# Performance work log

Hardware: AMD Instinct MI355X
Metric: run time of the kernel (lower is better)

The kernel has to match this reference:

```python
import jax, jax.numpy as jnp
import numpy as np

R_MAX = 5.0
NUM_RADIAL = 8
HIDDEN = 128
MUL1 = HIDDEN // 2  # multiplicity of the 1o irrep (l_max=1)
SILU_2MOM = 1.679177  # e3nn normalize2mom constant for silu
SQRT3 = 3.0 ** 0.5
N_NODES = 50000
N_EDGES = 400000


def setup_inputs():
    key = jax.random.key(0)
    ks = jax.random.split(key, 9)
    node_attrs = jax.random.normal(ks[0], (N_NODES, HIDDEN), jnp.float32)
    edge_index = jax.random.randint(ks[1], (2, N_EDGES), 0, N_NODES, jnp.int32)
    edge_vec = jax.random.normal(ks[2], (N_EDGES, 3), jnp.float32)
    edge_len = jax.random.uniform(ks[3], (N_EDGES,), jnp.float32, 0.05, R_MAX * 0.95)
    W1 = jax.random.normal(ks[4], (NUM_RADIAL, 64), jnp.float32)
    W2 = jax.random.normal(ks[5], (64, HIDDEN), jnp.float32)
    Wtp0 = jax.random.normal(ks[6], (HIDDEN, HIDDEN), jnp.float32)  # 0e x 0e -> 0e path weights
    Wtp1 = jax.random.normal(ks[7], (HIDDEN, MUL1), jnp.float32)   # 0e x 1o -> 1o path weights
    Wmix0 = jax.random.normal(ks[8], (HIDDEN + MUL1, HIDDEN), jnp.float32)  # o3.Linear 0e->0e
    return dict(node_attrs=node_attrs, edge_index=edge_index, edge_vec=edge_vec,
                edge_len=edge_len, W1=W1, W2=W2, Wtp0=Wtp0, Wtp1=Wtp1, Wmix0=Wmix0)


def _ace_forward(node_attrs, edge_vec, edge_len, W1, W2, Wtp0, Wtp1, Wmix0, sender, receiver):
    N = node_attrs.shape[0]
    # --- bessel radial basis with cutoff (e3nn soft_one_hot_linspace, basis='bessel') ---
    roots = jnp.arange(1, NUM_RADIAL + 1, dtype=node_attrs.dtype) * jnp.pi
    x = edge_len[:, None]
    rad = jnp.sqrt(2.0 / R_MAX) * jnp.sin(roots * x / R_MAX) / x        # [E, num_radial]
    rad = rad * (((edge_len > 0.0) & (edge_len < R_MAX)).astype(rad.dtype))[:, None]
    # --- radial MLP (e3nn FullyConnectedNet: W/sqrt(fan_in), 2nd-moment-normalized silu) ---
    h = SILU_2MOM * jax.nn.silu(rad @ (W1 / np.sqrt(NUM_RADIAL)))
    R_n = h @ (W2 / np.sqrt(64.0))                                       # [E, H]
    # --- spherical harmonics l<=1, normalize=True, 'component' norm; e3nn l=1 order (y,z,x) ---
    unit = edge_vec / jnp.linalg.norm(edge_vec, axis=-1, keepdims=True)
    Y1 = SQRT3 * unit[:, jnp.array([1, 2, 0])]                           # [E, 3]; Y0 == 1
    # --- gather + radial gating ---
    node_feats = node_attrs[sender] * R_n                                # [E, H]
    # --- FullyConnectedTensorProduct: Hx0e (x) (1x0e+1x1o) -> Hx0e + (H/2)x1o ---
    # effective coefficient per path: alpha * w3j = 1/sqrt(fan_in) = 1/sqrt(H)
    inv = 1.0 / np.sqrt(HIDDEN)
    f0 = (node_feats @ Wtp0) * inv                                       # [E, H]
    f1 = (node_feats @ Wtp1)[:, :, None] * Y1[:, None, :] * inv         # [E, H/2, 3]
    edge_feats = jnp.concatenate([f0, f1.reshape(-1, 3 * MUL1)], axis=-1)  # [E, 320]
    # --- scatter-add over receivers -> atomic basis A ---
    A = jnp.zeros((N, HIDDEN + 3 * MUL1), edge_feats.dtype).at[receiver].add(edge_feats)
    A0 = A[:, :HIDDEN]                                                   # [N, H]   (0e)
    A1 = A[:, HIDDEN:].reshape(N, MUL1, 3)                               # [N, H/2, 3] (1o)
    # --- ElementwiseTensorProduct(A, A): only scalar channels feed mix ---
    # 0e x 0e -> 0e: A0*A0 ; 1o x 1o -> 0e: (a.a)/sqrt(3) (w3j * sqrt(2l+1));
    # 1o x 1o -> 1e is cross(A1, A1) == 0; -> 2e has no matching output irrep in mix.
    B0 = jnp.concatenate([A0 * A0, jnp.sum(A1 * A1, axis=-1) / SQRT3], axis=-1)  # [N, 192]
    # --- o3.Linear(contraction_out -> irreps_out): only 0e->0e path; 1o output is zero ---
    mix0 = B0 @ (Wmix0 / np.sqrt(HIDDEN + MUL1))                         # [N, H]
    # return mix(B_basis) + A_basis
    return A.at[:, :HIDDEN].add(mix0)


def reference(node_attrs, edge_index, edge_vec, edge_len, W1, W2, Wtp0, Wtp1, Wmix0):
    sender, receiver = edge_index[0], edge_index[1]
    return _ace_forward(node_attrs, edge_vec, edge_len, W1, W2, Wtp0, Wtp1, Wmix0, sender, receiver)
```

## Files before the change

kernel.cpp:

```cpp
#include <hip/hip_runtime.h>
#include <math.h>

#define HIDDEN 128
#define MUL1   64
#define ACOLS  320
#define TBINS  4096
#define NWAVES 16384

typedef unsigned short ushort_t;
typedef __attribute__((ext_vector_type(8))) _Float16 f16x8;
typedef __attribute__((ext_vector_type(4))) float f32x4;

__device__ __forceinline__ unsigned short f2h(float x) {
  return __builtin_bit_cast(unsigned short, (_Float16)x);
}
__device__ __forceinline__ unsigned pack2h(float a, float b) {
  return (unsigned)f2h(a) | ((unsigned)f2h(b) << 16);
}
__device__ __forceinline__ float hlo(unsigned u) {
  return (float)__builtin_bit_cast(_Float16, (unsigned short)(u & 0xffffu));
}
__device__ __forceinline__ float hhi(unsigned u) {
  return (float)__builtin_bit_cast(_Float16, (unsigned short)(u >> 16));
}

__global__ __launch_bounds__(128) void tab_hist(const float* __restrict__ W1,
                                                const float* __restrict__ W2,
                                                ushort_t* __restrict__ TqB,
                                                const int* __restrict__ recv,
                                                int* __restrict__ cnt, int n_edges,
                                                const float* __restrict__ attrs,
                                                unsigned* __restrict__ attrsB,
                                                int n2, int hist_blocks) {
  const int tid = threadIdx.x;
  if (blockIdx.x > TBINS) {
    const int hb = blockIdx.x - (TBINS + 1);
    if (hb < hist_blocks) {
      const int e = hb * 128 + tid;
      if (e < n_edges) atomicAdd(&cnt[recv[e]], 1);
    } else {
      const int i = (hb - hist_blocks) * 128 + tid;
      if (i < n2) {
        const float2 v = ((const float2*)attrs)[i];
        attrsB[i] = pack2h(v.x, v.y);
      }
    }
    return;
  }
  __shared__ float hsh[64];
  const int i = blockIdx.x;
  const float x = (float)i * (5.0f / TBINS);
  if (tid < 64) {
    const bool valid = (x > 0.0f) && (x < 5.0f);
    const float invx = valid ? (1.0f / x) : 0.0f;
    float z = 0.0f;
#pragma unroll
    for (int r = 0; r < 8; ++r) {
      float arg = (float)(r + 1) * 0.6283185307f * x;
      float rad = 0.6324555320f * sinf(arg) * invx;
      z += rad * (W1[r * 64 + tid] * 0.3535533906f);
    }
    float sg = 1.0f / (1.0f + expf(-z));
    hsh[tid] = 1.679177f * z * sg;
  }
  __syncthreads();
  float acc = 0.0f;
  for (int j = 0; j < 64; ++j)
    acc += hsh[j] * W2[j * HIDDEN + tid];
  acc *= 0.125f;
  const ushort_t a16 = f2h(acc);
  TqB[((size_t)i * HIDDEN + tid) * 2] = a16;
  if (i >= 1)
    TqB[((size_t)(i - 1) * HIDDEN + tid) * 2 + 1] = a16;
}

__global__ __launch_bounds__(1024) void scan_blocks(const int* __restrict__ cnt,
                                                    int* __restrict__ partial,
                                                    int* __restrict__ bsums, int n) {
  __shared__ int buf[1024];
  const int t = threadIdx.x;
  const int i = blockIdx.x * 1024 + t;
  const int v = (i < n) ? cnt[i] : 0;
  buf[t] = v;
  __syncthreads();
  for (int d = 1; d < 1024; d <<= 1) {
    const int x = buf[t];
    const int y = (t >= d) ? buf[t - d] : 0;
    __syncthreads();
    buf[t] = x + y;
    __syncthreads();
  }
  if (i < n) partial[i] = buf[t] - v;
  if (t == 1023) bsums[blockIdx.x] = buf[1023];
}

__global__ __launch_bounds__(1024) void scan_sums(int* __restrict__ bsums, int nb,
                                                  int* __restrict__ off, int n) {
  __shared__ int buf[1024];
  const int t = threadIdx.x;
  const int v = (t < nb) ? bsums[t] : 0;
  buf[t] = v;
  __syncthreads();
  for (int d = 1; d < 1024; d <<= 1) {
    const int x = buf[t];
    const int y = (t >= d) ? buf[t - d] : 0;
    __syncthreads();
    buf[t] = x + y;
    __syncthreads();
  }
  if (t < nb) bsums[t] = buf[t] - v;
  if (t == nb - 1) off[n] = buf[t];
}

__global__ __launch_bounds__(256) void scan_final(const int* __restrict__ partial,
                                                  const int* __restrict__ bsums,
                                                  int* __restrict__ off,
                                                  int* __restrict__ cur, int n) {
  const int i = blockIdx.x * 256 + threadIdx.x;
  if (i < n) {
    const int o = partial[i] + bsums[i >> 10];
    off[i] = o;
    cur[i] = o;
  }
}

__global__ __launch_bounds__(256) void scatter_kernel(
    const int* __restrict__ eidx, const float* __restrict__ evec,
    const float* __restrict__ elen, int* __restrict__ cur,
    float4* __restrict__ recs, int n_edges,
    const int* __restrict__ off, int* __restrict__ lb, int n_nodes,
    int edge_blocks) {
  if (blockIdx.x >= edge_blocks) {
    const int w = (blockIdx.x - edge_blocks) * 256 + threadIdx.x;
    if (w > NWAVES) return;
    if (w == NWAVES) { lb[w] = n_nodes; return; }
    const long long target = ((long long)w * (long long)n_edges) / NWAVES;
    int lo = 0, hi = n_nodes;
    while (lo < hi) {
      const int mid = (lo + hi) >> 1;
      if ((long long)off[mid] < target) lo = mid + 1; else hi = mid;
    }
    lb[w] = lo;
    return;
  }
  const int e = blockIdx.x * 256 + threadIdx.x;
  if (e >= n_edges) return;
  const int s = eidx[e], r = eidx[n_edges + e];
  const float x = elen[e];
  const float v0 = evec[3 * e], v1 = evec[3 * e + 1], v2 = evec[3 * e + 2];
  const float rn = rsqrtf(v0 * v0 + v1 * v1 + v2 * v2);
  const float u = x * ((float)TBINS / 5.0f);
  int i0 = (int)floorf(u);
  i0 = i0 < 0 ? 0 : (i0 > TBINS - 1 ? TBINS - 1 : i0);
  const float fr = u - (float)i0;
  const bool valid = (x > 0.0f) && (x < 5.0f);
  const float w0 = valid ? 1.0f - fr : 0.0f;
  const float w1 = valid ? fr : 0.0f;
  const int pos = atomicAdd(&cur[r], 1);
  recs[2 * pos]     = make_float4(__int_as_float(s), w0, w1, __int_as_float(i0));
  recs[2 * pos + 1] = make_float4(1.7320508076f * v1 * rn,
                                  1.7320508076f * v2 * rn,
                                  1.7320508076f * v0 * rn, 0.0f);
}

__global__ __launch_bounds__(256) void pack_weights(
    const float* __restrict__ W0, const float* __restrict__ W1,
    const float* __restrict__ Wm, ushort_t* __restrict__ P) {
  const int idx = blockIdx.x * 256 + threadIdx.x;
  const int j = idx & 7, lane = (idx >> 3) & 63;
  const int krow = (lane >> 4) * 8 + j, col = lane & 15;
  float v;
  if (idx < 16384) {
    const int tq = idx >> 9, nt = tq >> 2, q = tq & 3;
    v = W0[(krow + q * 32) * HIDDEN + nt * 16 + col] * 0.0883883476f;
  } else if (idx < 24576) {
    const int i2 = idx - 16384;
    const int tq = i2 >> 9, nt = tq >> 2, q = tq & 3;
    v = W1[(krow + q * 32) * MUL1 + nt * 16 + col] * 0.0883883476f;
  } else {
    const int i3 = idx - 24576;
    const int tq = i3 >> 9, nt = tq / 6, q = tq % 6;
    v = Wm[(krow + q * 32) * HIDDEN + nt * 16 + col] * 18.4752086f;
  }
  P[idx] = f2h(v);
}

__global__ __launch_bounds__(512) void node_sg(
    const unsigned* __restrict__ attrsB, const unsigned* __restrict__ TqB,
    const float4* __restrict__ recs, const int* __restrict__ off,
    const int* __restrict__ lb, unsigned* __restrict__ SG, int n_nodes) {
  const int lane = threadIdx.x & 63;
  const int wid = __builtin_amdgcn_readfirstlane((blockIdx.x << 3) +
                                                 (threadIdx.x >> 6));
  const int nbeg = lb[wid], nend = lb[wid + 1];
  const unsigned* tqb = TqB + 2 * lane;
  const unsigned* atb = attrsB + lane;
  for (int n = nbeg; n < nend; ++n) {
    const int beg = off[n], end = off[n + 1];
    const int cnt = end - beg;
    float Sa = 0.f, Sb = 0.f;
    float Ga0 = 0.f, Ga1 = 0.f, Ga2 = 0.f, Gb0 = 0.f, Gb1 = 0.f, Gb2 = 0.f;
    int i = beg;
    const int m8 = beg + (cnt & ~7);
    for (; i < m8; i += 8) {
      float4 ra[8], rb[8];
#pragma unroll
      for (int b = 0; b < 8; ++b) {
        ra[b] = recs[2 * (i + b)];
        rb[b] = recs[2 * (i + b) + 1];
      }
      uint2 tqv[8];
      unsigned avv[8];
#pragma unroll
      for (int b = 0; b < 8; ++b) {
        tqv[b] = *(const uint2*)(tqb + ((unsigned)__float_as_int(ra[b].w) << 7));
        avv[b] = atb[(unsigned)__float_as_int(ra[b].x) << 6];
      }
#pragma unroll
      for (int b = 0; b < 8; ++b) {
        const float Ra = ra[b].y * hlo(tqv[b].x) + ra[b].z * hhi(tqv[b].x);
        const float Rb = ra[b].y * hlo(tqv[b].y) + ra[b].z * hhi(tqv[b].y);
        const float la = hlo(avv[b]) * Ra, lb2 = hhi(avv[b]) * Rb;
        Sa += la; Sb += lb2;
        Ga0 += la * rb[b].x; Ga1 += la * rb[b].y; Ga2 += la * rb[b].z;
        Gb0 += lb2 * rb[b].x; Gb1 += lb2 * rb[b].y; Gb2 += lb2 * rb[b].z;
      }
    }
    const int m4 = beg + (cnt & ~3);
    for (; i < m4; i += 4) {
      float4 ra[4], rb[4];
#pragma unroll
      for (int b = 0; b < 4; ++b) {
        ra[b] = recs[2 * (i + b)];
        rb[b] = recs[2 * (i + b) + 1];
      }
      uint2 tqv[4];
      unsigned avv[4];
#pragma unroll
      for (int b = 0; b < 4; ++b) {
        tqv[b] = *(const uint2*)(tqb + ((unsigned)__float_as_int(ra[b].w) << 7));
        avv[b] = atb[(unsigned)__float_as_int(ra[b].x) << 6];
      }
#pragma unroll
      for (int b = 0; b < 4; ++b) {
        const float Ra = ra[b].y * hlo(tqv[b].x) + ra[b].z * hhi(tqv[b].x);
        const float Rb = ra[b].y * hlo(tqv[b].y) + ra[b].z * hhi(tqv[b].y);
        const float la = hlo(avv[b]) * Ra, lb2 = hhi(avv[b]) * Rb;
        Sa += la; Sb += lb2;
        Ga0 += la * rb[b].x; Ga1 += la * rb[b].y; Ga2 += la * rb[b].z;
        Gb0 += lb2 * rb[b].x; Gb1 += lb2 * rb[b].y; Gb2 += lb2 * rb[b].z;
      }
    }
    for (; i < end; ++i) {
      const float4 ra = recs[2 * i];
      const float4 rb = recs[2 * i + 1];
      const int s = __float_as_int(ra.x);
      const int i0 = __float_as_int(ra.w);
      const uint2 tq = *(const uint2*)(tqb + ((unsigned)i0 << 7));
      const unsigned av = atb[(unsigned)s << 6];
      const float Ra = ra.y * hlo(tq.x) + ra.z * hhi(tq.x);
      const float Rb = ra.y * hlo(tq.y) + ra.z * hhi(tq.y);
      const float la = hlo(av) * Ra, lb2 = hhi(av) * Rb;
      Sa += la; Sb += lb2;
      Ga0 += la * rb.x; Ga1 += la * rb.y; Ga2 += la * rb.z;
      Gb0 += lb2 * rb.x; Gb1 += lb2 * rb.y; Gb2 += lb2 * rb.z;
    }
    unsigned* srow = SG + (size_t)n * 256;
    srow[lane]       = pack2h(Sa, Sb);
    srow[64 + lane]  = pack2h(Ga0, Gb0);
    srow[128 + lane] = pack2h(Ga1, Gb1);
    srow[192 + lane] = pack2h(Ga2, Gb2);
  }
}

struct F3 { float x, y, z; };

__global__ __launch_bounds__(64, 2) void node_mfma(
    const ushort_t* __restrict__ SG, const ushort_t* __restrict__ P,
    float* __restrict__ out, int n_nodes) {
  __shared__ ushort_t B0s[16][200];
  const int lane = threadIdx.x & 63;
  const int tile = blockIdx.x;
  const int row = lane & 15, quad = lane >> 4;
  const int nA = min(tile * 16 + row, n_nodes - 1);
  const ushort_t* sgA = SG + (size_t)nA * 512;
  const int cnode0 = tile * 16 + quad * 4;

  const ushort_t* W0f = P;
  const ushort_t* W1f = P + 16384;
  const ushort_t* Wmf = P + 24576;

  f16x8 aS[4], aG[3][4];
#pragma unroll
  for (int q = 0; q < 4; ++q)
    aS[q] = *(const f16x8*)(sgA + quad * 8 + q * 32);
#pragma unroll
  for (int d = 0; d < 3; ++d)
#pragma unroll
    for (int q = 0; q < 4; ++q)
      aG[d][q] = *(const f16x8*)(sgA + 128 + d * 128 + quad * 8 + q * 32);

  f32x4 c0[8];
#pragma unroll
  for (int nt = 0; nt < 8; ++nt) c0[nt] = (f32x4){0.f, 0.f, 0.f, 0.f};
  f32x4 c1[3][4];
#pragma unroll
  for (int d = 0; d < 3; ++d)
#pragma unroll
    for (int nt = 0; nt < 4; ++nt) c1[d][nt] = (f32x4){0.f, 0.f, 0.f, 0.f};

  {
    f16x8 pb[3][4];
#pragma unroll
    for (int nt = 0; nt < 2; ++nt)
#pragma unroll
      for (int q = 0; q < 4; ++q)
        pb[nt][q] = *(const f16x8*)(W0f + ((nt * 4 + q) * 64 + lane) * 8);
#pragma unroll
    for (int nt = 0; nt < 8; ++nt) {
      const int cur = nt % 3;
      if (nt < 6) {
        const int dst = (nt + 2) % 3;
#pragma unroll
        for (int q = 0; q < 4; ++q)
          pb[dst][q] = *(const f16x8*)(W0f + (((nt + 2) * 4 + q) * 64 + lane) * 8);
      }
#pragma unroll
      for (int q = 0; q < 4; ++q)
        c0[nt] = __builtin_amdgcn_mfma_f32_16x16x32_f16(aS[q], pb[cur][q], c0[nt], 0, 0, 0);
    }
  }

  {
    f16x8 pb[3][4];
#pragma unroll
    for (int nt = 0; nt < 2; ++nt)
#pragma unroll
      for (int q = 0; q < 4; ++q)
        pb[nt][q] = *(const f16x8*)(W1f + ((nt * 4 + q) * 64 + lane) * 8);
#pragma unroll
    for (int nt = 0; nt < 4; ++nt) {
      const int cur = nt % 3;
      if (nt < 2) {
        const int dst = (nt + 2) % 3;
#pragma unroll
        for (int q = 0; q < 4; ++q)
          pb[dst][q] = *(const f16x8*)(W1f + (((nt + 2) * 4 + q) * 64 + lane) * 8);
      }
#pragma unroll
      for (int q = 0; q < 4; ++q)
#pragma unroll
        for (int d = 0; d < 3; ++d)
          c1[d][nt] = __builtin_amdgcn_mfma_f32_16x16x32_f16(aG[d][q], pb[cur][q], c1[d][nt], 0, 0, 0);
    }
  }

#pragma unroll
  for (int nt = 0; nt < 4; ++nt) {
    const int m = nt * 16 + row;
#pragma unroll
    for (int r = 0; r < 4; ++r) {
      const int n = cnode0 + r;
      if (n < n_nodes) {
        F3 v3 = {c1[0][nt][r], c1[1][nt][r], c1[2][nt][r]};
        *(F3*)&out[(size_t)n * ACOLS + HIDDEN + 3 * m] = v3;
      }
    }
  }

#pragma unroll
  for (int nt = 0; nt < 8; ++nt)
#pragma unroll
    for (int r = 0; r < 4; ++r) {
      const float a = c0[nt][r] * 0.0625f;
      B0s[quad * 4 + r][nt * 16 + row] = f2h(a * a);
    }
#pragma unroll
  for (int nt = 0; nt < 4; ++nt)
#pragma unroll
    for (int r = 0; r < 4; ++r) {
      const float x = c1[0][nt][r] * 0.0625f, y = c1[1][nt][r] * 0.0625f,
                  z = c1[2][nt][r] * 0.0625f;
      B0s[quad * 4 + r][HIDDEN + nt * 16 + row] =
          f2h((x * x + y * y + z * z) * 0.5773502692f);
    }

  f16x8 mh[3][8];
#pragma unroll
  for (int qq = 0; qq < 2; ++qq)
#pragma unroll
    for (int nt = 0; nt < 8; ++nt)
      mh[qq][nt] = *(const f16x8*)(Wmf + ((nt * 6 + qq) * 64 + lane) * 8);

  asm volatile("s_waitcnt lgkmcnt(0)" ::: "memory");
  __builtin_amdgcn_sched_barrier(0);

#pragma unroll
  for (int q = 0; q < 6; ++q) {
    const int cur = q % 3;
    if (q < 4) {
      const int dst = (q + 2) % 3;
#pragma unroll
      for (int nt = 0; nt < 8; ++nt)
        mh[dst][nt] = *(const f16x8*)(Wmf + ((nt * 6 + (q + 2)) * 64 + lane) * 8);
    }
    const f16x8 ah = *(const f16x8*)&B0s[row][quad * 8 + q * 32];
#pragma unroll
    for (int nt = 0; nt < 8; ++nt)
      c0[nt] = __builtin_amdgcn_mfma_f32_16x16x32_f16(ah, mh[cur][nt], c0[nt], 0, 0, 0);
  }

#pragma unroll
  for (int nt = 0; nt < 8; ++nt)
#pragma unroll
    for (int r = 0; r < 4; ++r) {
      const int n = cnode0 + r;
      if (n < n_nodes) out[(size_t)n * ACOLS + nt * 16 + row] = c0[nt][r];
    }
}

extern "C" void kernel_launch(void* const* d_in, const int* in_sizes, int n_in,
                              void* d_out, int out_size, void* d_ws, size_t ws_size,
                              hipStream_t stream) {
  const float* attrs = (const float*)d_in[0];
  const int*   eidx  = (const int*)d_in[1];
  const float* evec  = (const float*)d_in[2];
  const float* elen  = (const float*)d_in[3];
  const float* W1    = (const float*)d_in[4];
  const float* W2    = (const float*)d_in[5];
  const float* Wtp0  = (const float*)d_in[6];
  const float* Wtp1  = (const float*)d_in[7];
  const float* Wmix  = (const float*)d_in[8];
  float* out = (float*)d_out;

  const int n_nodes = in_sizes[0] / HIDDEN;
  const int n_edges = in_sizes[1] / 2;

  char* ws = (char*)d_ws;
  float4* recs = (float4*)ws;
  size_t o1 = (((size_t)n_edges * 32) + 255) & ~(size_t)255;
  ushort_t* TqB = (ushort_t*)(ws + o1);
  size_t o2 = (o1 + (size_t)(TBINS + 1) * HIDDEN * 4 + 255) & ~(size_t)255;
  int* cnt = (int*)(ws + o2);
  size_t o3 = (o2 + (size_t)n_nodes * 4 + 255) & ~(size_t)255;
  int* off = (int*)(ws + o3);
  size_t o4 = (o3 + (size_t)(n_nodes + 1) * 4 + 255) & ~(size_t)255;
  int* cur = (int*)(ws + o4);
  size_t o5 = (o4 + (size_t)n_nodes * 4 + 255) & ~(size_t)255;
  int* partial = (int*)(ws + o5);
  size_t o6 = (o5 + (size_t)n_nodes * 4 + 255) & ~(size_t)255;
  int* bsums = (int*)(ws + o6);
  size_t o6b = o6 + 1024 * 4;
  int* lb = (int*)(ws + o6b);
  size_t o7 = (o6b + (size_t)(NWAVES + 1) * 4 + 255) & ~(size_t)255;
  unsigned* SG = (unsigned*)(ws + o7);
  size_t o8 = o7 + (size_t)n_nodes * 1024;
  ushort_t* P = (ushort_t*)(ws + o8);
  size_t o9 = (o8 + 49152 * 2 + 255) & ~(size_t)255;
  unsigned* attrsB = (unsigned*)(ws + o9);

  (void)hipMemsetAsync(cnt, 0, (size_t)n_nodes * 4, stream);
  const int n2 = n_nodes * 64;
  const int hist_blocks = (n_edges + 127) / 128;
  const int pack_blocks = (n2 + 127) / 128;
  tab_hist<<<TBINS + 1 + hist_blocks + pack_blocks, 128, 0, stream>>>(
      W1, W2, TqB, eidx + n_edges, cnt, n_edges, attrs, attrsB, n2, hist_blocks);
  const int nscan = (n_nodes + 1023) / 1024;
  scan_blocks<<<nscan, 1024, 0, stream>>>(cnt, partial, bsums, n_nodes);
  scan_sums<<<1, 1024, 0, stream>>>(bsums, nscan, off, n_nodes);
  scan_final<<<(n_nodes + 255) / 256, 256, 0, stream>>>(partial, bsums, off, cur,
                                                        n_nodes);
  const int edge_blocks = (n_edges + 255) / 256;
  const int wb_blocks = (NWAVES + 1 + 255) / 256;
  scatter_kernel<<<edge_blocks + wb_blocks, 256, 0, stream>>>(
      eidx, evec, elen, cur, recs, n_edges, off, lb, n_nodes, edge_blocks);
  pack_weights<<<192, 256, 0, stream>>>(Wtp0, Wtp1, Wmix, P);
  node_sg<<<2048, 512, 0, stream>>>(attrsB, (const unsigned*)TqB, recs, off, lb,
                                    SG, n_nodes);
  const int ntiles = (n_nodes + 15) / 16;
  node_mfma<<<ntiles, 64, 0, stream>>>((const ushort_t*)SG, P, out, n_nodes);
}
```

Baseline: 222.4 us.

## Compress edge records to 16 bytes and fold weight packing into tab_hist

Edge records shrink from two float4s (32 B) to one uint4 (16 B). The sender index goes into 16 bits, the table bin into 16 bits, and the interpolation weights and unit vector are stored as fp16. This halves the record traffic written by scatter_kernel and read by node_sg. The weight-packing kernel is merged into tab_hist to save a launch, and attrs packing is widened to float4. The 16-bit sender index only holds for node counts up to 65536, and fp16 weights and directions lower precision.

After: 214.2 us. 3.7% less time.

```diff
diff --git a/kernel.cpp b/kernel.cpp
--- a/kernel.cpp
+++ b/kernel.cpp
@@ -24,25 +24,46 @@
   return (float)__builtin_bit_cast(_Float16, (unsigned short)(u >> 16));
 }
 
-__global__ __launch_bounds__(128) void tab_hist(const float* __restrict__ W1,
-                                                const float* __restrict__ W2,
-                                                ushort_t* __restrict__ TqB,
-                                                const int* __restrict__ recv,
-                                                int* __restrict__ cnt, int n_edges,
-                                                const float* __restrict__ attrs,
-                                                unsigned* __restrict__ attrsB,
-                                                int n2, int hist_blocks) {
+__global__ __launch_bounds__(128) void tab_hist(
+    const float* __restrict__ W1, const float* __restrict__ W2,
+    ushort_t* __restrict__ TqB, const int* __restrict__ recv,
+    int* __restrict__ cnt, int n_edges,
+    const float* __restrict__ attrs, unsigned* __restrict__ attrsB, int n4,
+    const float* __restrict__ Wtp0, const float* __restrict__ Wtp1,
+    const float* __restrict__ Wmix, ushort_t* __restrict__ P,
+    int hist_blocks, int apack_blocks) {
   const int tid = threadIdx.x;
   if (blockIdx.x > TBINS) {
     const int hb = blockIdx.x - (TBINS + 1);
     if (hb < hist_blocks) {
       const int e = hb * 128 + tid;
       if (e < n_edges) atomicAdd(&cnt[recv[e]], 1);
+    } else if (hb < hist_blocks + apack_blocks) {
+      const int i = (hb - hist_blocks) * 128 + tid;
+      if (i < n4) {
+        const float4 v = ((const float4*)attrs)[i];
+        uint2 o; o.x = pack2h(v.x, v.y); o.y = pack2h(v.z, v.w);
+        ((uint2*)attrsB)[i] = o;
+      }
     } else {
-      const int i = (hb - hist_blocks) * 128 + tid;
-      if (i < n2) {
-        const float2 v = ((const float2*)attrs)[i];
-        attrsB[i] = pack2h(v.x, v.y);
+      const int idx = (hb - hist_blocks - apack_blocks) * 128 + tid;
+      if (idx < 49152) {
+        const int j = idx & 7, lane = (idx >> 3) & 63;
+        const int krow = (lane >> 4) * 8 + j, col = lane & 15;
+        float v;
+        if (idx < 16384) {
+          const int tq = idx >> 9, nt = tq >> 2, q = tq & 3;
+          v = Wtp0[(krow + q * 32) * HIDDEN + nt * 16 + col] * 0.0883883476f;
+        } else if (idx < 24576) {
+          const int i2 = idx - 16384;
+          const int tq = i2 >> 9, nt = tq >> 2, q = tq & 3;
+          v = Wtp1[(krow + q * 32) * MUL1 + nt * 16 + col] * 0.0883883476f;
+        } else {
+          const int i3 = idx - 24576;
+          const int tq = i3 >> 9, nt = tq / 6, q = tq % 6;
+          v = Wmix[(krow + q * 32) * HIDDEN + nt * 16 + col] * 18.4752086f;
+        }
+        P[idx] = f2h(v);
       }
     }
     return;
@@ -127,7 +148,7 @@
 __global__ __launch_bounds__(256) void scatter_kernel(
     const int* __restrict__ eidx, const float* __restrict__ evec,
     const float* __restrict__ elen, int* __restrict__ cur,
-    float4* __restrict__ recs, int n_edges,
+    uint4* __restrict__ recs, int n_edges,
     const int* __restrict__ off, int* __restrict__ lb, int n_nodes,
     int edge_blocks) {
   if (blockIdx.x >= edge_blocks) {
@@ -157,37 +178,17 @@
   const float w0 = valid ? 1.0f - fr : 0.0f;
   const float w1 = valid ? fr : 0.0f;
   const int pos = atomicAdd(&cur[r], 1);
-  recs[2 * pos]     = make_float4(__int_as_float(s), w0, w1, __int_as_float(i0));
-  recs[2 * pos + 1] = make_float4(1.7320508076f * v1 * rn,
-                                  1.7320508076f * v2 * rn,
-                                  1.7320508076f * v0 * rn, 0.0f);
-}
-
-__global__ __launch_bounds__(256) void pack_weights(
-    const float* __restrict__ W0, const float* __restrict__ W1,
-    const float* __restrict__ Wm, ushort_t* __restrict__ P) {
-  const int idx = blockIdx.x * 256 + threadIdx.x;
-  const int j = idx & 7, lane = (idx >> 3) & 63;
-  const int krow = (lane >> 4) * 8 + j, col = lane & 15;
-  float v;
-  if (idx < 16384) {
-    const int tq = idx >> 9, nt = tq >> 2, q = tq & 3;
-    v = W0[(krow + q * 32) * HIDDEN + nt * 16 + col] * 0.0883883476f;
-  } else if (idx < 24576) {
-    const int i2 = idx - 16384;
-    const int tq = i2 >> 9, nt = tq >> 2, q = tq & 3;
-    v = W1[(krow + q * 32) * MUL1 + nt * 16 + col] * 0.0883883476f;
-  } else {
-    const int i3 = idx - 24576;
-    const int tq = i3 >> 9, nt = tq / 6, q = tq % 6;
-    v = Wm[(krow + q * 32) * HIDDEN + nt * 16 + col] * 18.4752086f;
-  }
-  P[idx] = f2h(v);
+  uint4 rec;
+  rec.x = (unsigned)(s & 0xFFFF) | ((unsigned)i0 << 16);
+  rec.y = pack2h(w0, w1);
+  rec.z = pack2h(1.7320508076f * v1 * rn, 1.7320508076f * v2 * rn);
+  rec.w = pack2h(1.7320508076f * v0 * rn, 0.0f);
+  recs[pos] = rec;
 }
 
 __global__ __launch_bounds__(512) void node_sg(
     const unsigned* __restrict__ attrsB, const unsigned* __restrict__ TqB,
-    const float4* __restrict__ recs, const int* __restrict__ off,
+    const uint4* __restrict__ recs, const int* __restrict__ off,
     const int* __restrict__ lb, unsigned* __restrict__ SG, int n_nodes) {
   const int lane = threadIdx.x & 63;
   const int wid = __builtin_amdgcn_readfirstlane((blockIdx.x << 3) +
@@ -203,67 +204,70 @@
     int i = beg;
     const int m8 = beg + (cnt & ~7);
     for (; i < m8; i += 8) {
-      float4 ra[8], rb[8];
-#pragma unroll
-      for (int b = 0; b < 8; ++b) {
-        ra[b] = recs[2 * (i + b)];
-        rb[b] = recs[2 * (i + b) + 1];
-      }
+      uint4 rc[8];
+#pragma unroll
+      for (int b = 0; b < 8; ++b) rc[b] = recs[i + b];
       uint2 tqv[8];
       unsigned avv[8];
 #pragma unroll
       for (int b = 0; b < 8; ++b) {
-        tqv[b] = *(const uint2*)(tqb + ((unsigned)__float_as_int(ra[b].w) << 7));
-        avv[b] = atb[(unsigned)__float_as_int(ra[b].x) << 6];
+        const unsigned sv = rc[b].x & 0xFFFFu;
+        const unsigned i0 = rc[b].x >> 16;
+        tqv[b] = *(const uint2*)(tqb + (i0 << 7));
+        avv[b] = atb[sv << 6];
       }
 #pragma unroll
       for (int b = 0; b < 8; ++b) {
-        const float Ra = ra[b].y * hlo(tqv[b].x) + ra[b].z * hhi(tqv[b].x);
-        const float Rb = ra[b].y * hlo(tqv[b].y) + ra[b].z * hhi(tqv[b].y);
+        const float w0 = hlo(rc[b].y), w1 = hhi(rc[b].y);
+        const float Ra = w0 * hlo(tqv[b].x) + w1 * hhi(tqv[b].x);
+        const float Rb = w0 * hlo(tqv[b].y) + w1 * hhi(tqv[b].y);
         const float la = hlo(avv[b]) * Ra, lb2 = hhi(avv[b]) * Rb;
+        const float r0 = hlo(rc[b].z), r1 = hhi(rc[b].z), r2 = hlo(rc[b].w);
         Sa += la; Sb += lb2;
-        Ga0 += la * rb[b].x; Ga1 += la * rb[b].y; Ga2 += la * rb[b].z;
-        Gb0 += lb2 * rb[b].x; Gb1 += lb2 * rb[b].y; Gb2 += lb2 * rb[b].z;
+        Ga0 += la * r0; Ga1 += la * r1; Ga2 += la * r2;
+        Gb0 += lb2 * r0; Gb1 += lb2 * r1; Gb2 += lb2 * r2;
       }
     }
     const int m4 = beg + (cnt & ~3);
     for (; i < m4; i += 4) {
-      float4 ra[4], rb[4];
-#pragma unroll
-      for (int b = 0; b < 4; ++b) {
-        ra[b] = recs[2 * (i + b)];
-        rb[b] = recs[2 * (i + b) + 1];
-      }
+      uint4 rc[4];
+#pragma unroll
+      for (int b = 0; b < 4; ++b) rc[b] = recs[i + b];
       uint2 tqv[4];
       unsigned avv[4];
 #pragma unroll
       for (int b = 0; b < 4; ++b) {
-        tqv[b] = *(const uint2*)(tqb + ((unsigned)__float_as_int(ra[b].w) << 7));
-        avv[b] = atb[(unsigned)__float_as_int(ra[b].x) << 6];
+        const unsigned sv = rc[b].x & 0xFFFFu;
+        const unsigned i0 = rc[b].x >> 16;
+        tqv[b] = *(const uint2*)(tqb + (i0 << 7));
+        avv[b] = atb[sv << 6];
       }
 #pragma unroll
       for (int b = 0; b < 4; ++b) {
-        const float Ra = ra[b].y * hlo(tqv[b].x) + ra[b].z * hhi(tqv[b].x);
-        const float Rb = ra[b].y * hlo(tqv[b].y) + ra[b].z * hhi(tqv[b].y);
+        const float w0 = hlo(rc[b].y), w1 = hhi(rc[b].y);
+        const float Ra = w0 * hlo(tqv[b].x) + w1 * hhi(tqv[b].x);
+        const float Rb = w0 * hlo(tqv[b].y) + w1 * hhi(tqv[b].y);
         const float la = hlo(avv[b]) * Ra, lb2 = hhi(avv[b]) * Rb;
+        const float r0 = hlo(rc[b].z), r1 = hhi(rc[b].z), r2 = hlo(rc[b].w);
         Sa += la; Sb += lb2;
-        Ga0 += la * rb[b].x; Ga1 += la * rb[b].y; Ga2 += la * rb[b].z;
-        Gb0 += lb2 * rb[b].x; Gb1 += lb2 * rb[b].y; Gb2 += lb2 * rb[b].z;
+        Ga0 += la * r0; Ga1 += la * r1; Ga2 += la * r2;
+        Gb0 += lb2 * r0; Gb1 += lb2 * r1; Gb2 += lb2 * r2;
       }
     }
     for (; i < end; ++i) {
-      const float4 ra = recs[2 * i];
-      const float4 rb = recs[2 * i + 1];
-      const int s = __float_as_int(ra.x);
-      const int i0 = __float_as_int(ra.w);
-      const uint2 tq = *(const uint2*)(tqb + ((unsigned)i0 << 7));
-      const unsigned av = atb[(unsigned)s << 6];
-      const float Ra = ra.y * hlo(tq.x) + ra.z * hhi(tq.x);
-      const float Rb = ra.y * hlo(tq.y) + ra.z * hhi(tq.y);
+      const uint4 rc = recs[i];
+      const unsigned sv = rc.x & 0xFFFFu;
+      const unsigned i0 = rc.x >> 16;
+      const uint2 tq = *(const uint2*)(tqb + (i0 << 7));
+      const unsigned av = atb[sv << 6];
+      const float w0 = hlo(rc.y), w1 = hhi(rc.y);
+      const float Ra = w0 * hlo(tq.x) + w1 * hhi(tq.x);
+      const float Rb = w0 * hlo(tq.y) + w1 * hhi(tq.y);
       const float la = hlo(av) * Ra, lb2 = hhi(av) * Rb;
+      const float r0 = hlo(rc.z), r1 = hhi(rc.z), r2 = hlo(rc.w);
       Sa += la; Sb += lb2;
-      Ga0 += la * rb.x; Ga1 += la * rb.y; Ga2 += la * rb.z;
-      Gb0 += lb2 * rb.x; Gb1 += lb2 * rb.y; Gb2 += lb2 * rb.z;
+      Ga0 += la * r0; Ga1 += la * r1; Ga2 += la * r2;
+      Gb0 += lb2 * r0; Gb1 += lb2 * r1; Gb2 += lb2 * r2;
     }
     unsigned* srow = SG + (size_t)n * 256;
     srow[lane]       = pack2h(Sa, Sb);
@@ -437,8 +441,8 @@
   const int n_edges = in_sizes[1] / 2;
 
   char* ws = (char*)d_ws;
-  float4* recs = (float4*)ws;
-  size_t o1 = (((size_t)n_edges * 32) + 255) & ~(size_t)255;
+  uint4* recs = (uint4*)ws;
+  size_t o1 = (((size_t)n_edges * 16) + 255) & ~(size_t)255;
   ushort_t* TqB = (ushort_t*)(ws + o1);
   size_t o2 = (o1 + (size_t)(TBINS + 1) * HIDDEN * 4 + 255) & ~(size_t)255;
   int* cnt = (int*)(ws + o2);
@@ -460,11 +464,13 @@
   unsigned* attrsB = (unsigned*)(ws + o9);
 
   (void)hipMemsetAsync(cnt, 0, (size_t)n_nodes * 4, stream);
-  const int n2 = n_nodes * 64;
+  const int n4 = n_nodes * 32;
   const int hist_blocks = (n_edges + 127) / 128;
-  const int pack_blocks = (n2 + 127) / 128;
-  tab_hist<<<TBINS + 1 + hist_blocks + pack_blocks, 128, 0, stream>>>(
-      W1, W2, TqB, eidx + n_edges, cnt, n_edges, attrs, attrsB, n2, hist_blocks);
+  const int apack_blocks = (n4 + 127) / 128;
+  const int wpack_blocks = (49152 + 127) / 128;
+  tab_hist<<<TBINS + 1 + hist_blocks + apack_blocks + wpack_blocks, 128, 0,
+             stream>>>(W1, W2, TqB, eidx + n_edges, cnt, n_edges, attrs, attrsB,
+                       n4, Wtp0, Wtp1, Wmix, P, hist_blocks, apack_blocks);
   const int nscan = (n_nodes + 1023) / 1024;
   scan_blocks<<<nscan, 1024, 0, stream>>>(cnt, partial, bsums, n_nodes);
   scan_sums<<<1, 1024, 0, stream>>>(bsums, nscan, off, n_nodes);
@@ -474,7 +480,6 @@
   const int wb_blocks = (NWAVES + 1 + 255) / 256;
   scatter_kernel<<<edge_blocks + wb_blocks, 256, 0, stream>>>(
       eidx, evec, elen, cur, recs, n_edges, off, lb, n_nodes, edge_blocks);
-  pack_weights<<<192, 256, 0, stream>>>(Wtp0, Wtp1, Wmix, P);
   node_sg<<<2048, 512, 0, stream>>>(attrsB, (const unsigned*)TqB, recs, off, lb,
                                     SG, n_nodes);
   const int ntiles = (n_nodes + 15) / 16;
```
